# Optimization experiments

Measured on AMD Instinct MI355X. Metric: run time of the kernel, lower is better.

Reference implementation:

```python
import jax, jax.numpy as jnp
import numpy as np

B, S, I, H, L, O = 32, 512, 1024, 1024, 3, 1024


def setup_inputs() -> dict:
    key = jax.random.key(0)
    ks = jax.random.split(key, 13)
    sc = 1.0 / np.sqrt(H)
    w = lambda k, shape: (jax.random.normal(k, shape, dtype=jnp.float32) * sc)
    return {
        "x": jax.random.normal(ks[0], (B, S, I), dtype=jnp.float32),
        "h0": jax.random.normal(ks[1], (B, L, H), dtype=jnp.float32),
        "Wzi": w(ks[2], (L, H, I)),
        "Wzh": w(ks[3], (L, H, H)),
        "bzh": w(ks[4], (L, H)),
        "Wri": w(ks[5], (L, H, I)),
        "Wrh": w(ks[6], (L, H, H)),
        "brh": w(ks[7], (L, H)),
        "Wgi": w(ks[8], (L, H, I)),
        "Wgh": w(ks[9], (L, H, H)),
        "bgh": w(ks[10], (L, H)),
        "Wout": w(ks[11], (O, H)),
        "bout": w(ks[12], (O,)),
    }


def reference(x, h0, Wzi, Wzh, bzh, Wri, Wrh, brh, Wgi, Wgh, bgh, Wout, bout):
    n_layers = Wzi.shape[0]
    # carry: hidden per layer, shape (L, B, H)
    h_init = jnp.transpose(h0, (1, 0, 2))
    x_t_major = jnp.transpose(x, (1, 0, 2))  # (S, B, I)

    def step(h, x_t):
        inp = x_t
        new_h = []
        for l in range(n_layers):
            hl = h[l]
            z = jax.nn.sigmoid(inp @ Wzi[l].T + hl @ Wzh[l].T + bzh[l])
            r = jax.nn.sigmoid(inp @ Wri[l].T + hl @ Wrh[l].T + brh[l])
            g = jnp.tanh(inp @ Wgi[l].T + r * (hl @ Wgh[l].T + bgh[l]))
            hn = z * hl + (1.0 - z) * g  # update gate keeps old state
            new_h.append(hn)
            inp = hn
        out_t = inp @ Wout.T + bout
        return jnp.stack(new_h), out_t

    h_final, outs = jax.lax.scan(step, h_init, x_t_major)
    layer_output = jnp.transpose(outs, (1, 0, 2))   # (B, S, O)
    hidden_state = jnp.transpose(h_final, (1, 0, 2))  # (B, L, H)
    return layer_output, hidden_state
```

## Files before the change

### kernel.cpp

```cpp
#include <hip/hip_runtime.h>
#include <hip/hip_bf16.h>


#define NB 32
#define NS 512
#define NI 1024
#define NH 1024
#define NL 3
#define NO 1024

#define WGN 256
#define BLK 512
#define SLOTS 12
#define RPB 2096
#define ZROW 72
#define COFF (73 * RPB)
#define CPITCH 33
#define LDSB (COFF + 48 * CPITCH * 4)

using short8 = __attribute__((ext_vector_type(8))) short;
using floatx4 = __attribute__((ext_vector_type(4))) float;

static __device__ __forceinline__ float bf2f(unsigned short u) {
    union { unsigned int i; float f; } v;
    v.i = ((unsigned int)u) << 16;
    return v.f;
}

static __device__ __forceinline__ unsigned short f2bf(float f) {
    __hip_bfloat16 h = __float2bfloat16(f);
    union { __hip_bfloat16 h; unsigned short u; } v;
    v.h = h;
    return v.u;
}

static __device__ __forceinline__ void load8h(const unsigned short* p, float w[8]) {
    uint4 q = *(const uint4*)p;
    unsigned int u[4] = {q.x, q.y, q.z, q.w};
#pragma unroll
    for (int i = 0; i < 4; ++i) {
        w[2*i]   = __uint_as_float(u[i] << 16);
        w[2*i+1] = __uint_as_float(u[i] & 0xffff0000u);
    }
}

static __device__ __forceinline__ void load8f(const float* p, float w[8]) {
    float4 a = *(const float4*)p;
    float4 b = *(const float4*)(p + 4);
    w[0]=a.x; w[1]=a.y; w[2]=a.z; w[3]=a.w;
    w[4]=b.x; w[5]=b.y; w[6]=b.z; w[7]=b.w;
}

__global__ void detect_kernel(const unsigned int* __restrict__ xw, int* __restrict__ flag) {
    __shared__ int cnt[256];
    int c = 0;
    for (int i = threadIdx.x; i < 1024; i += 256) {
        unsigned int e = (xw[i] >> 7) & 0xFFu;
        if (e >= 0x78u && e <= 0x84u) c++;
    }
    cnt[threadIdx.x] = c;
    __syncthreads();
    if (threadIdx.x == 0) {
        int s = 0;
        for (int i = 0; i < 256; ++i) s += cnt[i];
        *flag = (s < 512) ? 1 : 0;
    }
}

__global__ void init_act(const void* __restrict__ h0,
                         unsigned int* __restrict__ act,
                         unsigned int* __restrict__ gflags,
                         const int* __restrict__ flagp) {
    const int f32m = *flagp;
    const int idx = blockIdx.x * 256 + threadIdx.x;
    if (idx < WGN * 32 + 32) gflags[idx] = 0u;
    if (idx >= NL * NB * NH) return;
    const int l = idx >> 15;
    const int b = (idx >> 10) & 31;
    const int j = idx & 1023;
    const size_t src = (size_t)b * NL * NH + (size_t)l * NH + j;
    float v = f32m ? ((const float*)h0)[src] : bf2f(((const unsigned short*)h0)[src]);
    unsigned short hi = f2bf(v);
    unsigned short lo = f2bf(v - bf2f(hi));
    const size_t dst = ((size_t)(l * 2 + 1) * NB + b) * NH + j;
    act[dst] = ((unsigned int)hi << 16) | lo;
}

__global__ __launch_bounds__(BLK, 2) void gru_persist(
    const void* __restrict__ x,
    const void* __restrict__ Wzi_, const void* __restrict__ Wzh_, const void* __restrict__ bzh_,
    const void* __restrict__ Wri_, const void* __restrict__ Wrh_, const void* __restrict__ brh_,
    const void* __restrict__ Wgi_, const void* __restrict__ Wgh_, const void* __restrict__ bgh_,
    void* __restrict__ dout,
    unsigned int* __restrict__ act,
    float* __restrict__ stfin,
    const int* __restrict__ flagp,
    unsigned int* __restrict__ gflags)
{
    extern __shared__ char lds[];
    float* clds = (float*)(lds + COFF);

    const int f32m = *flagp;
    const int tid  = threadIdx.x;
    const int wg   = blockIdx.x;
    const int lane = tid & 63;
    const int wid  = tid >> 6;
    const int Mtile = wid & 1;
    const int khalf = wid >> 1;
    const int n16  = lane & 15;
    const int q4   = lane >> 4;

    const int slot0 = wg * SLOTS;

    {
        const void* Wmats[6] = {Wzi_, Wzh_, Wri_, Wrh_, Wgi_, Wgh_};
        if (f32m) {
            for (int idx = tid; idx < 72 * 256; idx += BLK) {
                const int r = idx >> 8, c4 = (idx & 255) * 4;
                const int slot = slot0 + r / 6, g = r % 6;
                const int layer = slot >> 10, j = slot & 1023;
                const float* src = (const float*)Wmats[g] + (size_t)layer * NH * NI + (size_t)j * NI + c4;
                float4 f = *(const float4*)src;
                unsigned short* dst = (unsigned short*)(lds + r * RPB + c4 * 2);
                dst[0] = f2bf(f.x); dst[1] = f2bf(f.y); dst[2] = f2bf(f.z); dst[3] = f2bf(f.w);
            }
        } else {
            for (int idx = tid; idx < 72 * 128; idx += BLK) {
                const int r = idx >> 7, c8 = (idx & 127) * 8;
                const int slot = slot0 + r / 6, g = r % 6;
                const int layer = slot >> 10, j = slot & 1023;
                const unsigned short* src = (const unsigned short*)Wmats[g] + (size_t)layer * NH * NI + (size_t)j * NI + c8;
                *(uint4*)(lds + r * RPB + c8 * 2) = *(const uint4*)src;
            }
        }
        unsigned int* z = (unsigned int*)(lds + ZROW * RPB);
        for (int c = tid; c < RPB / 4; c += BLK) z[c] = 0u;
    }

    int eci = 0, eb = 0, elg = 0, ej = 0;
    float ebz = 0.f, ebr = 0.f, ebg = 0.f, ehp = 0.f;
    if (tid < NB * SLOTS) {
        eci = tid % SLOTS; eb = tid / SLOTS;
        const int slot = slot0 + eci;
        elg = slot >> 10; ej = slot & 1023;
        const size_t bidx = (size_t)elg * NH + ej;
        if (f32m) {
            ebz = ((const float*)bzh_)[bidx];
            ebr = ((const float*)brh_)[bidx];
            ebg = ((const float*)bgh_)[bidx];
        } else {
            ebz = bf2f(((const unsigned short*)bzh_)[bidx]);
            ebr = bf2f(((const unsigned short*)brh_)[bidx]);
            ebg = bf2f(((const unsigned short*)bgh_)[bidx]);
        }
    }

    const int lay0 = slot0 >> 10;
    const int lay1 = (slot0 + SLOTS - 1) >> 10;
    const int ngroups = (lay0 == lay1) ? 1 : 2;
    const int n0 = (ngroups == 1) ? SLOTS : (1024 - (slot0 & 1023));

    __syncthreads();

    for (int s = 0; s < NS + NL - 1; ++s) {
        for (int i = tid; i < 48 * CPITCH; i += BLK) clds[i] = 0.f;
        __syncthreads();

        floatx4 acc[3];
#pragma unroll
        for (int nt = 0; nt < 3; ++nt) acc[nt] = (floatx4){0.f, 0.f, 0.f, 0.f};

        for (int grp = 0; grp < ngroups; ++grp) {
            const int lg = (grp == 0) ? lay0 : lay1;
            const int t = s - lg;
            if (t < 0 || t >= NS) continue;
            const int ntLo = (grp == 0) ? 0 : ((4 * n0) >> 4);
            const int ntHi = (grp == 0) ? (ngroups == 1 ? 2 : ((4 * n0) >> 4) - 1) : 2;
            const int mb = Mtile * 16 + n16;

            for (int phase = 0; phase < 2; ++phase) {
                int brow[3];
#pragma unroll
                for (int nt = 0; nt < 3; ++nt) {
                    const int v = nt * 16 + n16;
                    const int ci = v >> 2, g = v & 3;
                    int r;
                    if (phase == 0) r = (g == 3) ? ZROW : ci * 6 + ((g == 2) ? 4 : g * 2);
                    else            r = (g == 2) ? ZROW : ci * 6 + ((g == 3) ? 5 : g * 2 + 1);
                    brow[nt] = r;
                }

                const bool isx = (phase == 0 && lg == 0);
                const bool dolo = isx ? (f32m != 0) : true;

                short8 AH[8], AL[8];
                if (isx) {
                    if (f32m) {
                        const float* xb = (const float*)x + ((size_t)mb * NS + t) * NI + khalf * 256 + q4 * 8;
#pragma unroll
                        for (int ks = 0; ks < 8; ++ks) {
                            float f[8];
                            load8f(xb + ks * 32, f);
#pragma unroll
                            for (int e = 0; e < 8; ++e) {
                                unsigned short h = f2bf(f[e]);
                                AH[ks][e] = (short)h;
                                AL[ks][e] = (short)f2bf(f[e] - bf2f(h));
                            }
                        }
                    } else {
                        const unsigned short* xb = (const unsigned short*)x + ((size_t)mb * NS + t) * NI + khalf * 256 + q4 * 8;
#pragma unroll
                        for (int ks = 0; ks < 8; ++ks)
                            AH[ks] = *(const short8*)(xb + ks * 32);
                    }
                } else {
                    const int src_l = (phase == 0) ? lg - 1 : lg;
                    const int src_p = (phase == 0) ? (t & 1) : ((t - 1) & 1);
                    const size_t ab = ((size_t)(src_l * 2 + src_p) * NB + mb) * NH + khalf * 256 + q4 * 8;
                    const uint4* ap = (const uint4*)(act + ab);
                    uint4 qq[16];
#pragma unroll
                    for (int ks = 0; ks < 8; ++ks) {
                        qq[2*ks]   = ap[ks * 8];
                        qq[2*ks+1] = ap[ks * 8 + 1];
                    }
#pragma unroll
                    for (int ks = 0; ks < 8; ++ks) {
                        unsigned int c[8] = {qq[2*ks].x, qq[2*ks].y, qq[2*ks].z, qq[2*ks].w,
                                             qq[2*ks+1].x, qq[2*ks+1].y, qq[2*ks+1].z, qq[2*ks+1].w};
#pragma unroll
                        for (int e = 0; e < 8; ++e) {
                            AH[ks][e] = (short)(c[e] >> 16);
                            AL[ks][e] = (short)(c[e] & 0xffffu);
                        }
                    }
                }

#pragma unroll
                for (int ks = 0; ks < 8; ++ks) {
                    const int k0 = khalf * 256 + ks * 32;
#pragma unroll
                    for (int nt = 0; nt < 3; ++nt) {
                        if (nt < ntLo || nt > ntHi) continue;
                        const short8 bf = *(const short8*)(lds + brow[nt] * RPB + k0 * 2 + q4 * 16);
                        acc[nt] = __builtin_amdgcn_mfma_f32_16x16x32_bf16(AH[ks], bf, acc[nt], 0, 0, 0);
                        if (dolo)
                            acc[nt] = __builtin_amdgcn_mfma_f32_16x16x32_bf16(AL[ks], bf, acc[nt], 0, 0, 0);
                    }
                }
            }
        }

        {
            const int mbase = Mtile * 16 + q4 * 4;
#pragma unroll
            for (int nt = 0; nt < 3; ++nt) {
                const int vcol = nt * 16 + n16;
#pragma unroll
                for (int r = 0; r < 4; ++r)
                    atomicAdd(&clds[vcol * CPITCH + mbase + r], acc[nt][r]);
            }
        }
        __syncthreads();

        if (tid < NB * SLOTS) {
            const int t = s - elg;
            if (t >= 0 && t < NS) {
                const float zp = clds[(eci * 4 + 0) * CPITCH + eb];
                const float rp = clds[(eci * 4 + 1) * CPITCH + eb];
                const float gi = clds[(eci * 4 + 2) * CPITCH + eb];
                const float gh = clds[(eci * 4 + 3) * CPITCH + eb];
                float hp;
                if (t == 0) {
                    const size_t hoff = ((size_t)(elg * 2 + 1) * NB + eb) * NH + ej;
                    const unsigned int pv = act[hoff];
                    hp = bf2f((unsigned short)(pv >> 16)) + bf2f((unsigned short)(pv & 0xffffu));
                } else {
                    hp = ehp;
                }
                const float z = 1.f / (1.f + expf(-(zp + ebz)));
                const float r = 1.f / (1.f + expf(-(rp + ebr)));
                const float g = tanhf(gi + r * (gh + ebg));
                const float hn = z * hp + (1.f - z) * g;
                ehp = hn;
                const unsigned short hi = f2bf(hn);
                const unsigned short lo = f2bf(hn - bf2f(hi));
                const size_t woff = ((size_t)(elg * 2 + (t & 1)) * NB + eb) * NH + ej;
                __hip_atomic_store(&act[woff], ((unsigned int)hi << 16) | lo,
                                   __ATOMIC_RELAXED, __HIP_MEMORY_SCOPE_AGENT);
                if (elg == 2) {
                    const size_t o = ((size_t)eb * NS + t) * NO + ej;
                    if (f32m) ((float*)dout)[o] = hn;
                    else      ((unsigned short*)dout)[o] = f2bf(hn);
                }
                if (t == NS - 1)
                    stfin[((size_t)elg * NB + eb) * NH + ej] = hn;
            }
        }

        __syncthreads();
        if (tid == 0)
            __hip_atomic_store(&gflags[wg * 32], (unsigned int)(s + 1),
                               __ATOMIC_RELAXED, __HIP_MEMORY_SCOPE_AGENT);
        if (wg == 0) {
            if (tid < WGN) {
                while (__hip_atomic_load(&gflags[tid * 32], __ATOMIC_RELAXED,
                                         __HIP_MEMORY_SCOPE_AGENT) <= (unsigned int)s)
                    __builtin_amdgcn_s_sleep(2);
            }
            __syncthreads();
            if (tid == 0) {
                __hip_atomic_store(&gflags[WGN * 32], (unsigned int)(s + 1),
                                   __ATOMIC_RELAXED, __HIP_MEMORY_SCOPE_AGENT);
                __builtin_amdgcn_fence(__ATOMIC_ACQUIRE, "agent");
            }
            __syncthreads();
        } else {
            if (tid == 0) {
                while (__hip_atomic_load(&gflags[WGN * 32], __ATOMIC_RELAXED,
                                         __HIP_MEMORY_SCOPE_AGENT) <= (unsigned int)s)
                    __builtin_amdgcn_s_sleep(2);
                __builtin_amdgcn_fence(__ATOMIC_ACQUIRE, "agent");
            }
            __syncthreads();
        }
    }
}

__global__ void init_kernel(const void* __restrict__ h0, float* __restrict__ st,
                            const int* __restrict__ flagp) {
    const int f32m = *flagp;
    const int idx = blockIdx.x * 256 + threadIdx.x;
    if (idx >= NL * NB * NH) return;
    const int l = idx >> 15;
    const int b = (idx >> 10) & 31;
    const int j = idx & 1023;
    const size_t src = (size_t)b * NL * NH + (size_t)l * NH + j;
    st[idx] = f32m ? ((const float*)h0)[src] : bf2f(((const unsigned short*)h0)[src]);
}

__global__ __launch_bounds__(256) void gru_layer(
    const void*  __restrict__ x,
    const float* __restrict__ inp,
    const float* __restrict__ hprev,
    float*       __restrict__ hnew,
    void*        __restrict__ h2out,
    const void* __restrict__ Wzi_, const void* __restrict__ Wzh_, const void* __restrict__ bzh_,
    const void* __restrict__ Wri_, const void* __restrict__ Wrh_, const void* __restrict__ brh_,
    const void* __restrict__ Wgi_, const void* __restrict__ Wgh_, const void* __restrict__ bgh_,
    const int* __restrict__ flagp, int tl, int isX)
{
    __shared__ float s_in[NB][129];
    __shared__ float s_h [NB][129];
    __shared__ float s_red[256][6];

    const int f32m = *flagp;
    const int t = tl & 0xFFFF;
    const int l = tl >> 16;
    const int tid = threadIdx.x;
    const int b   = tid & 31;
    const int jl  = (tid >> 5) & 1;
    const int ks  = tid >> 6;
    const int j   = blockIdx.x * 2 + jl;

    const size_t wIl = (size_t)l * NH * NI + (size_t)j * NI;
    const size_t bl  = (size_t)l * NH + j;

    float azi = 0.f, azh = 0.f, ari = 0.f, arh = 0.f, agi = 0.f, agh = 0.f;

    for (int kc = 0; kc < 8; ++kc) {
        const int k0 = kc * 128;
        __syncthreads();
        for (int idx = tid; idx < NB * 128; idx += 256) {
            const int r = idx >> 7, c = idx & 127;
            float vi;
            if (isX) {
                const size_t xo = (size_t)r * NS * NI + (size_t)t * NI + (k0 + c);
                vi = f32m ? ((const float*)x)[xo] : bf2f(((const unsigned short*)x)[xo]);
            } else {
                vi = inp[r * NH + k0 + c];
            }
            s_in[r][c] = vi;
            s_h [r][c] = hprev[r * NH + k0 + c];
        }
        __syncthreads();

        const int cbase = ks * 32;
#pragma unroll
        for (int q8 = 0; q8 < 4; ++q8) {
            const int c = cbase + q8 * 8;
            const int k = k0 + c;
            float wz[8], wr[8], wg[8], vz[8], vr[8], vg[8];
            if (f32m) {
                load8f((const float*)Wzi_ + wIl + k, wz);
                load8f((const float*)Wri_ + wIl + k, wr);
                load8f((const float*)Wgi_ + wIl + k, wg);
                load8f((const float*)Wzh_ + wIl + k, vz);
                load8f((const float*)Wrh_ + wIl + k, vr);
                load8f((const float*)Wgh_ + wIl + k, vg);
            } else {
                load8h((const unsigned short*)Wzi_ + wIl + k, wz);
                load8h((const unsigned short*)Wri_ + wIl + k, wr);
                load8h((const unsigned short*)Wgi_ + wIl + k, wg);
                load8h((const unsigned short*)Wzh_ + wIl + k, vz);
                load8h((const unsigned short*)Wrh_ + wIl + k, vr);
                load8h((const unsigned short*)Wgh_ + wIl + k, vg);
            }
            float ai[8], ah[8];
#pragma unroll
            for (int q = 0; q < 8; ++q) { ai[q] = s_in[b][c + q]; ah[q] = s_h[b][c + q]; }
#pragma unroll
            for (int q = 0; q < 8; ++q) {
                azi = fmaf(wz[q], ai[q], azi);
                ari = fmaf(wr[q], ai[q], ari);
                agi = fmaf(wg[q], ai[q], agi);
                azh = fmaf(vz[q], ah[q], azh);
                arh = fmaf(vr[q], ah[q], arh);
                agh = fmaf(vg[q], ah[q], agh);
            }
        }
    }

    s_red[tid][0] = azi; s_red[tid][1] = azh; s_red[tid][2] = ari;
    s_red[tid][3] = arh; s_red[tid][4] = agi; s_red[tid][5] = agh;
    __syncthreads();

    if (ks == 0) {
#pragma unroll
        for (int w = 1; w < 4; ++w) {
            azi += s_red[tid + 64*w][0]; azh += s_red[tid + 64*w][1];
            ari += s_red[tid + 64*w][2]; arh += s_red[tid + 64*w][3];
            agi += s_red[tid + 64*w][4]; agh += s_red[tid + 64*w][5];
        }
        const float bz = f32m ? ((const float*)bzh_)[bl] : bf2f(((const unsigned short*)bzh_)[bl]);
        const float br = f32m ? ((const float*)brh_)[bl] : bf2f(((const unsigned short*)brh_)[bl]);
        const float bg = f32m ? ((const float*)bgh_)[bl] : bf2f(((const unsigned short*)bgh_)[bl]);
        const float z = 1.f / (1.f + expf(-(azi + azh + bz)));
        const float r = 1.f / (1.f + expf(-(ari + arh + br)));
        const float g = tanhf(agi + r * (agh + bg));
        const float hp = hprev[b * NH + j];
        const float hn = z * hp + (1.f - z) * g;
        hnew[b * NH + j] = hn;
        if (h2out) {
            const size_t off = (size_t)b * NS * NO + (size_t)t * NO + j;
            if (f32m) ((float*)h2out)[off] = hn;
            else      ((unsigned short*)h2out)[off] = f2bf(hn);
        }
    }
}

__global__ __launch_bounds__(256) void out_gemm(
    void* __restrict__ out, const void* __restrict__ Wout, const void* __restrict__ bout,
    const int* __restrict__ flagp)
{
    __shared__ float s_a[8][1024];
    const int f32m = *flagp;
    const int tid = threadIdx.x;
    const size_t row0 = (size_t)blockIdx.x * 8;

    for (int idx = tid; idx < 8 * 1024; idx += 256) {
        const int r = idx >> 10, c = idx & 1023;
        const size_t off = (row0 + r) * NO + c;
        s_a[r][c] = f32m ? ((const float*)out)[off] : bf2f(((const unsigned short*)out)[off]);
    }
    __syncthreads();

    float acc[4][8];
#pragma unroll
    for (int m = 0; m < 4; ++m)
#pragma unroll
        for (int r = 0; r < 8; ++r) acc[m][r] = 0.f;

    for (int k8 = 0; k8 < 128; ++k8) {
        const int k = k8 * 8;
        float wf[4][8];
#pragma unroll
        for (int m = 0; m < 4; ++m) {
            const size_t wo = (size_t)(tid + 256*m) * NH + k;
            if (f32m) load8f((const float*)Wout + wo, wf[m]);
            else      load8h((const unsigned short*)Wout + wo, wf[m]);
        }
#pragma unroll
        for (int r = 0; r < 8; ++r) {
            float a[8];
#pragma unroll
            for (int q = 0; q < 8; ++q) a[q] = s_a[r][k + q];
#pragma unroll
            for (int m = 0; m < 4; ++m)
#pragma unroll
                for (int q = 0; q < 8; ++q)
                    acc[m][r] = fmaf(wf[m][q], a[q], acc[m][r]);
        }
    }

#pragma unroll
    for (int m = 0; m < 4; ++m) {
        const int jj = tid + 256*m;
        const float bj = f32m ? ((const float*)bout)[jj] : bf2f(((const unsigned short*)bout)[jj]);
#pragma unroll
        for (int r = 0; r < 8; ++r) {
            const size_t off = (row0 + r) * NO + jj;
            const float v = acc[m][r] + bj;
            if (f32m) ((float*)out)[off] = v;
            else      ((unsigned short*)out)[off] = f2bf(v);
        }
    }
}

__global__ void tail_kernel(const float* __restrict__ st, void* __restrict__ out,
                            const int* __restrict__ flagp)
{
    const int f32m = *flagp;
    const int idx = blockIdx.x * 256 + threadIdx.x;
    if (idx >= NL * NB * NH) return;
    const int l = idx >> 15;
    const int b = (idx >> 10) & 31;
    const int j = idx & 1023;
    const size_t dst = (size_t)NB * NS * NO + (size_t)b * NL * NH + (size_t)l * NH + j;
    if (f32m) ((float*)out)[dst] = st[idx];
    else      ((unsigned short*)out)[dst] = f2bf(st[idx]);
}

extern "C" void kernel_launch(void* const* d_in, const int* in_sizes, int n_in,
                              void* d_out, int out_size, void* d_ws, size_t ws_size,
                              hipStream_t stream)
{
    const void* x    = d_in[0];
    const void* h0   = d_in[1];
    const void* Wzi  = d_in[2];
    const void* Wzh  = d_in[3];
    const void* bzh  = d_in[4];
    const void* Wri  = d_in[5];
    const void* Wrh  = d_in[6];
    const void* brh  = d_in[7];
    const void* Wgi  = d_in[8];
    const void* Wgh  = d_in[9];
    const void* bgh  = d_in[10];
    const void* Wout = d_in[11];
    const void* bout = d_in[12];

    char* w = (char*)d_ws;
    float* st            = (float*)w;
    int*   flag          = (int*)(w + 786432);
    unsigned int* act    = (unsigned int*)(w + 786464);
    unsigned int* gflags = (unsigned int*)(w + 1572992);
    auto stp = [&](int p, int l) { return st + ((size_t)(p * NL + l)) * NB * NH; };

    detect_kernel<<<1, 256, 0, stream>>>((const unsigned int*)x, flag);
    init_act<<<(NL*NB*NH + 255)/256, 256, 0, stream>>>(h0, act, gflags, flag);

    (void)hipFuncSetAttribute((const void*)gru_persist,
                              hipFuncAttributeMaxDynamicSharedMemorySize, LDSB);
    (void)hipGetLastError();
    gru_persist<<<WGN, BLK, LDSB, stream>>>(
        x, Wzi, Wzh, bzh, Wri, Wrh, brh, Wgi, Wgh, bgh,
        d_out, act, st , flag, gflags);
    hipError_t perr = hipGetLastError();

    if (perr != hipSuccess) {
        init_kernel<<<(NL*NB*NH + 255)/256, 256, 0, stream>>>(h0, st, flag);
        for (int t = 0; t < NS; ++t) {
            const int pr = t & 1, pw = 1 - pr;
            for (int l = 0; l < NL; ++l) {
                gru_layer<<<512, 256, 0, stream>>>(
                    x,
                    l == 0 ? st : stp(pw, l - 1),
                    stp(pr, l),
                    stp(pw, l),
                    l == 2 ? d_out : (void*)nullptr,
                    Wzi, Wzh, bzh, Wri, Wrh, brh, Wgi, Wgh, bgh,
                    flag, t | (l << 16), l == 0 ? 1 : 0);
            }
        }
    }

    out_gemm<<<NB * NS / 8, 256, 0, stream>>>(d_out, Wout, bout, flag);
    tail_kernel<<<(NL*NB*NH + 255)/256, 256, 0, stream>>>(st, d_out, flag);
}
```

Before: 14.25 ms.

## Replace global barrier release with per-XCD claim and L2 invalidate protocol

Reworks the per-timestep grid barrier in the persistent GRU kernel. The single release flag becomes 16 separate generation flags, so fewer workgroups poll the same cache line. The agent-scope acquire fence now runs once per XCD: the first workgroup to claim the slot does the fence, and the others wait on a done flag and then do a cheaper buffer_inv. The sleep interval is also halved. The claim/done handshake adds atomics and relies on hardware-specific coherence behaviour, which risks subtle memory-ordering bugs.

```diff
diff --git a/kernel.cpp b/kernel.cpp
--- a/kernel.cpp
+++ b/kernel.cpp
@@ -18,6 +18,11 @@
 #define CPITCH 33
 #define LDSB (COFF + 48 * CPITCH * 4)
 
+#define GENB   (WGN * 32)
+#define CLAIMB (GENB + 16 * 32)
+#define DONEB  (CLAIMB + 16 * 32)
+#define GFL_N  9472
+
 using short8 = __attribute__((ext_vector_type(8))) short;
 using floatx4 = __attribute__((ext_vector_type(4))) float;
 
@@ -49,6 +54,12 @@
     float4 b = *(const float4*)(p + 4);
     w[0]=a.x; w[1]=a.y; w[2]=a.z; w[3]=a.w;
     w[4]=b.x; w[5]=b.y; w[6]=b.z; w[7]=b.w;
+}
+
+static __device__ __forceinline__ int xcc_id() {
+    unsigned v;
+    asm volatile("s_getreg_b32 %0, hwreg(20, 0, 32)" : "=s"(v));
+    return (int)(v & 7);
 }
 
 __global__ void detect_kernel(const unsigned int* __restrict__ xw, int* __restrict__ flag) {
@@ -73,7 +84,7 @@
                          const int* __restrict__ flagp) {
     const int f32m = *flagp;
     const int idx = blockIdx.x * 256 + threadIdx.x;
-    if (idx < WGN * 32 + 32) gflags[idx] = 0u;
+    if (idx < GFL_N) gflags[idx] = 0u;
     if (idx >= NL * NB * NH) return;
     const int l = idx >> 15;
     const int b = (idx >> 10) & 31;
@@ -159,6 +170,8 @@
     const int lay1 = (slot0 + SLOTS - 1) >> 10;
     const int ngroups = (lay0 == lay1) ? 1 : 2;
     const int n0 = (ngroups == 1) ? SLOTS : (1024 - (slot0 & 1023));
+
+    const int myxcd = xcc_id();
 
     __syncthreads();
 
@@ -307,24 +320,37 @@
             if (tid < WGN) {
                 while (__hip_atomic_load(&gflags[tid * 32], __ATOMIC_RELAXED,
                                          __HIP_MEMORY_SCOPE_AGENT) <= (unsigned int)s)
-                    __builtin_amdgcn_s_sleep(2);
+                    __builtin_amdgcn_s_sleep(1);
             }
             __syncthreads();
-            if (tid == 0) {
-                __hip_atomic_store(&gflags[WGN * 32], (unsigned int)(s + 1),
+            if (tid < 16)
+                __hip_atomic_store(&gflags[GENB + tid * 32], (unsigned int)(s + 1),
                                    __ATOMIC_RELAXED, __HIP_MEMORY_SCOPE_AGENT);
-                __builtin_amdgcn_fence(__ATOMIC_ACQUIRE, "agent");
-            }
-            __syncthreads();
         } else {
             if (tid == 0) {
-                while (__hip_atomic_load(&gflags[WGN * 32], __ATOMIC_RELAXED,
+                while (__hip_atomic_load(&gflags[GENB + (wg >> 4) * 32], __ATOMIC_RELAXED,
                                          __HIP_MEMORY_SCOPE_AGENT) <= (unsigned int)s)
-                    __builtin_amdgcn_s_sleep(2);
+                    __builtin_amdgcn_s_sleep(1);
+            }
+        }
+        if (tid == 0) {
+            const unsigned tag = (unsigned)(s + 1);
+            unsigned* claim = &gflags[CLAIMB + (myxcd * 2 + (s & 1)) * 32];
+            unsigned old = __hip_atomic_exchange(claim, tag,
+                                                 __ATOMIC_RELAXED, __HIP_MEMORY_SCOPE_AGENT);
+            if (old != tag) {
                 __builtin_amdgcn_fence(__ATOMIC_ACQUIRE, "agent");
-            }
-            __syncthreads();
-        }
+                __hip_atomic_store(&gflags[DONEB + myxcd * 32], tag,
+                                   __ATOMIC_RELAXED, __HIP_MEMORY_SCOPE_AGENT);
+            } else {
+                while (__hip_atomic_load(&gflags[DONEB + myxcd * 32], __ATOMIC_RELAXED,
+                                         __HIP_MEMORY_SCOPE_AGENT) <= (unsigned int)s)
+                    __builtin_amdgcn_s_sleep(1);
+                asm volatile("buffer_inv" ::: "memory");
+            }
+            __builtin_amdgcn_sched_barrier(0);
+        }
+        __syncthreads();
     }
 }
 
```

Result: faster. 13.63 ms (-4.4%).
